# Kernel optimization log

Measured on AMD Instinct MI355X. Metric: run time of the kernel, lower is better.

Reference implementation:

```python
import jax, jax.numpy as jnp
import numpy as np

H, D = 4, 32            # heads, per-head dim (hidden = H*D = 128)
HID = H * D
OUT = 64
NC, ND, E = 50000, 50000, 400000
FC, FD = 256, 256


def setup_inputs() -> dict:
    key = jax.random.key(0)
    ks = iter(jax.random.split(key, 64))

    def n(shape, s=0.05):
        return jax.random.normal(next(ks), shape, dtype=jnp.float32) * s

    def ei(n_src, n_dst):
        return jnp.stack([jax.random.randint(next(ks), (E,), 0, n_src),
                          jax.random.randint(next(ks), (E,), 0, n_dst)]).astype(jnp.int32)

    inp = {
        'x_concept': n((NC, FC), 1.0),
        'x_doc': n((ND, FD), 1.0),
        'ei_cc': ei(NC, NC),
        'ei_dc': ei(ND, NC),
        'ei_cd': ei(NC, ND),
        # conv1 params
        'W1c': n((FC, HID)), 'b1c': n((HID,)),
        'W1d': n((FD, HID)), 'b1d': n((HID,)),
        'a1s_cc': n((H, D)), 'a1d_cc': n((H, D)),
        'a1s_dc': n((H, D)), 'a1d_dc': n((H, D)),
        'a1s_cd': n((H, D)), 'a1d_cd': n((H, D)),
        'k1W': n((HID, HID)), 'k1b': n((HID,)), 'q1': n((HID,)),
        # conv2 params
        'W2c': n((HID, HID)), 'b2c': n((HID,)),
        'W2d': n((HID, HID)), 'b2d': n((HID,)),
        'a2s_cc': n((H, D)), 'a2d_cc': n((H, D)),
        'a2s_dc': n((H, D)), 'a2d_dc': n((H, D)),
        'a2s_cd': n((H, D)), 'a2d_cd': n((H, D)),
        'k2W': n((HID, HID)), 'k2b': n((HID,)), 'q2': n((HID,)),
        # final projection
        'pW': n((HID, OUT)), 'pb': n((OUT,)),
    }
    return inp


def _seg_softmax(logit, idx, n):
    # PyG softmax: exp(x - max_per_segment) / (sum_per_segment + 1e-16)
    m = jax.ops.segment_max(logit, idx, num_segments=n)
    e = jnp.exp(logit - m[idx])
    s = jax.ops.segment_sum(e, idx, num_segments=n)
    return e / (s[idx] + 1e-16)


def _edge_att(h_src, h_dst, a_s, a_d, src, dst, n_dst):
    # h_src: [Ns,H,D]; GAT-style per-edge attention, softmax over dst
    logit = jax.nn.leaky_relu((h_src * a_s).sum(-1)[src] + (h_dst * a_d).sum(-1)[dst], 0.2)
    alpha = _seg_softmax(logit, dst, n_dst)                     # [E,H]
    out = jax.ops.segment_sum(h_src[src] * alpha[:, :, None], dst, num_segments=n_dst)
    return jax.nn.relu(out.reshape(n_dst, H * D))


def _group(outs, kW, kb, q):
    # semantic attention across relation types
    stk = jnp.stack(outs)                                       # [T,N,C]
    score = (q * jnp.tanh(stk @ kW + kb).mean(axis=1)).sum(-1)  # [T]
    w = jax.nn.softmax(score)
    return jnp.einsum('t,tnc->nc', w, stk)


def _han_layer(xc, xd, Wc, bc, Wd, bd, as_cc, ad_cc, as_dc, ad_dc, as_cd, ad_cd,
               kW, kb, q, ei_cc, ei_dc, ei_cd):
    hc = (xc @ Wc + bc).reshape(-1, H, D)
    hd = (xd @ Wd + bd).reshape(-1, H, D)
    nc, nd = hc.shape[0], hd.shape[0]
    o_cc = _edge_att(hc, hc, as_cc, ad_cc, ei_cc[0], ei_cc[1], nc)
    o_dc = _edge_att(hd, hc, as_dc, ad_dc, ei_dc[0], ei_dc[1], nc)
    o_cd = _edge_att(hc, hd, as_cd, ad_cd, ei_cd[0], ei_cd[1], nd)
    return _group([o_cc, o_dc], kW, kb, q), _group([o_cd], kW, kb, q)


def reference(x_concept, x_doc, ei_cc, ei_dc, ei_cd,
              W1c, b1c, W1d, b1d, a1s_cc, a1d_cc, a1s_dc, a1d_dc, a1s_cd, a1d_cd, k1W, k1b, q1,
              W2c, b2c, W2d, b2d, a2s_cc, a2d_cc, a2s_dc, a2d_dc, a2s_cd, a2d_cd, k2W, k2b, q2,
              pW, pb):
    c, d = _han_layer(x_concept, x_doc, W1c, b1c, W1d, b1d,
                      a1s_cc, a1d_cc, a1s_dc, a1d_dc, a1s_cd, a1d_cd,
                      k1W, k1b, q1, ei_cc, ei_dc, ei_cd)
    c, d = jax.nn.elu(c), jax.nn.elu(d)
    c, d = _han_layer(c, d, W2c, b2c, W2d, b2d,
                      a2s_cc, a2d_cc, a2s_dc, a2d_dc, a2s_cd, a2d_cd,
                      k2W, k2b, q2, ei_cc, ei_dc, ei_cd)
    c, d = jax.nn.elu(c), jax.nn.elu(d)
    pc = c @ pW + pb
    pd = d @ pW + pb
    # F.normalize(p=2) on 'concept' only
    pc = pc / jnp.maximum(jnp.linalg.norm(pc, axis=-1, keepdims=True), 1e-12)
    return pc, pd
```

## Files before the change

### kernel.cpp

```cpp
#include <hip/hip_runtime.h>
#include <hip/hip_fp16.h>
#include <cmath>

#define DEVI static __device__ __forceinline__

constexpr int HIDn = 128, OUTn = 64;
constexpr int NCn = 50000, NDn = 50000, En = 400000;
constexpr int SCAN_N = 150000, SCAN_BLK = 1024;
constexpr int SCAN_NB = (SCAN_N + SCAN_BLK - 1) / SCAN_BLK;

typedef __attribute__((ext_vector_type(8))) short bf16x8;
typedef __attribute__((ext_vector_type(4))) float f32x4;

DEVI unsigned fmap(float f) {
  int i = __float_as_int(f);
  return (i < 0) ? ~((unsigned)i) : (((unsigned)i) | 0x80000000u);
}
DEVI float fdecode(unsigned u) {
  int i = (u & 0x80000000u) ? (int)(u & 0x7fffffffu) : (int)(~u);
  return __int_as_float(i);
}

DEVI float tanh_fast(float x) {
  float e = __expf(2.f * x);
  return 1.f - __fdividef(2.f, e + 1.f);
}

DEVI unsigned short f2bf(float x) {
  unsigned u = __float_as_uint(x);
  return (unsigned short)((u + 0x7FFFu + ((u >> 16) & 1u)) >> 16);
}
DEVI float bf2f(unsigned short h) {
  unsigned u = ((unsigned)h) << 16;
  return __uint_as_float(u);
}

template<int MODE, int HALF>
DEVI void loadrow8(float* __restrict__ tmp,
                   const void* __restrict__ A, const void* __restrict__ A2,
                   float w2, float w3, size_t base)
{
  float v[8];
  if (HALF) {
    float4 raw = *(const float4*)((const __half*)A + base);
    const __half2* h2 = (const __half2*)&raw;
    #pragma unroll
    for (int j = 0; j < 4; ++j) {
      float2 f = __half22float2(h2[j]);
      v[2 * j] = f.x; v[2 * j + 1] = f.y;
    }
  } else {
    const float4* p = (const float4*)((const float*)A + base);
    float4 u0 = p[0], u1 = p[1];
    v[0] = u0.x; v[1] = u0.y; v[2] = u0.z; v[3] = u0.w;
    v[4] = u1.x; v[5] = u1.y; v[6] = u1.z; v[7] = u1.w;
  }
  if (MODE == 2) {
    float vb[8];
    if (HALF) {
      float4 raw = *(const float4*)((const __half*)A2 + base);
      const __half2* h2 = (const __half2*)&raw;
      #pragma unroll
      for (int j = 0; j < 4; ++j) {
        float2 f = __half22float2(h2[j]);
        vb[2 * j] = f.x; vb[2 * j + 1] = f.y;
      }
    } else {
      const float4* q = (const float4*)((const float*)A2 + base);
      float4 t0 = q[0], t1 = q[1];
      vb[0] = t0.x; vb[1] = t0.y; vb[2] = t0.z; vb[3] = t0.w;
      vb[4] = t1.x; vb[5] = t1.y; vb[6] = t1.z; vb[7] = t1.w;
    }
    #pragma unroll
    for (int i = 0; i < 8; ++i) v[i] = w2 * v[i] + w3 * vb[i];
  }
  if (MODE >= 1) {
    #pragma unroll
    for (int i = 0; i < 8; ++i) v[i] = (v[i] > 0.f) ? v[i] : (__expf(v[i]) - 1.f);
  }
  #pragma unroll
  for (int i = 0; i < 8; ++i) tmp[i] = v[i];
}

template<int MODE, int HALF>
DEVI bf16x8 packrow8(const void* __restrict__ A, const void* __restrict__ A2,
                     float w2, float w3, size_t base)
{
  float t[8];
  loadrow8<MODE, HALF>(t, A, A2, w2, w3, base);
  bf16x8 r;
  #pragma unroll
  for (int i = 0; i < 8; ++i) r[i] = (short)f2bf(t[i]);
  return r;
}

template<int KI, int MODEc, int MODEd, int IN16, int OUT16>
__global__ __launch_bounds__(256)
void gemm2_mfma(const void* __restrict__ Ac, const void* __restrict__ Ac2,
                const float* __restrict__ wv,
                const unsigned short* __restrict__ WcH, const unsigned short* __restrict__ WcL,
                const float* __restrict__ bc, void* __restrict__ Cc,
                const void* __restrict__ Ad,
                const unsigned short* __restrict__ WdH, const unsigned short* __restrict__ WdL,
                const float* __restrict__ bd, void* __restrict__ Cd,
                int N,
                const float* __restrict__ avc0, const float* __restrict__ avc1,
                const float* __restrict__ avc2, const float* __restrict__ avc3,
                const float* __restrict__ avd0, const float* __restrict__ avd1,
                float* __restrict__ doc0, float* __restrict__ doc1,
                float* __restrict__ doc2, float* __restrict__ doc3,
                float* __restrict__ dod0, float* __restrict__ dod1)
{
  __shared__ float As[64][44];
  __shared__ unsigned short BhS[4096];
  __shared__ unsigned short BlS[4096];
  constexpr int NC = KI / 32;
  const bool isC = (blockIdx.y == 0);
  const void* A  = isC ? Ac : Ad;
  const void* A2 = isC ? Ac2 : nullptr;
  const unsigned short* WH = isC ? WcH : WdH;
  const unsigned short* WL = isC ? WcL : WdL;
  const float* bias = isC ? bc : bd;
  void* Cv = isC ? Cc : Cd;
  float w2 = 0.f, w3 = 0.f;
  if (MODEc == 2) { if (isC) { w2 = wv[2]; w3 = wv[3]; } }

  const int tid = threadIdx.x;
  const int w = tid >> 6, lane = tid & 63;
  const int m = lane & 15, b4 = lane >> 4;
  const int row0 = blockIdx.x * 64;
  const int row0w = row0 + w * 16;

  const int rA = tid >> 2, kqA = (tid & 3) << 3;
  const int rowA = row0 + rA;

  f32x4 acc[8];
  #pragma unroll
  for (int t = 0; t < 8; ++t) acc[t] = (f32x4){0.f, 0.f, 0.f, 0.f};

  float tA[8];
  float4 rbh0, rbh1, rbl0, rbl1;

  auto loadA = [&](int k0) {
    if (rowA < N) {
      if (isC) loadrow8<MODEc, IN16>(tA, A, A2, w2, w3, (size_t)rowA * KI + k0 + kqA);
      else     loadrow8<MODEd, IN16>(tA, A, nullptr, 0.f, 0.f, (size_t)rowA * KI + k0 + kqA);
    } else {
      #pragma unroll
      for (int i = 0; i < 8; ++i) tA[i] = 0.f;
    }
  };
  auto loadB = [&](int c) {
    const float4* ph = (const float4*)(WH + (size_t)c * 4096 + tid * 16);
    const float4* pl = (const float4*)(WL + (size_t)c * 4096 + tid * 16);
    rbh0 = ph[0]; rbh1 = ph[1];
    rbl0 = pl[0]; rbl1 = pl[1];
  };

  loadA(0);
  loadB(0);

  for (int c = 0; c < NC; ++c) {
    *(float4*)&As[rA][kqA]     = make_float4(tA[0], tA[1], tA[2], tA[3]);
    *(float4*)&As[rA][kqA + 4] = make_float4(tA[4], tA[5], tA[6], tA[7]);
    *(float4*)&BhS[tid * 16]     = rbh0;
    *(float4*)&BhS[tid * 16 + 8] = rbh1;
    *(float4*)&BlS[tid * 16]     = rbl0;
    *(float4*)&BlS[tid * 16 + 8] = rbl1;

    if (c + 1 < NC) { loadA((c + 1) * 32); loadB(c + 1); }
    __syncthreads();

    bf16x8 ah, al;
    {
      const float* ap = &As[w * 16 + m][b4 * 8];
      float4 u0 = *(const float4*)ap;
      float4 u1 = *(const float4*)(ap + 4);
      float t8[8] = {u0.x, u0.y, u0.z, u0.w, u1.x, u1.y, u1.z, u1.w};
      #pragma unroll
      for (int i = 0; i < 8; ++i) {
        unsigned short h = f2bf(t8[i]);
        ah[i] = (short)h;
        al[i] = (short)f2bf(t8[i] - bf2f(h));
      }
    }
    #pragma unroll
    for (int t = 0; t < 8; ++t) {
      const int fi = (t * 64 + lane) * 8;
      bf16x8 bh = *(const bf16x8*)&BhS[fi];
      bf16x8 bl = *(const bf16x8*)&BlS[fi];
      acc[t] = __builtin_amdgcn_mfma_f32_16x16x32_bf16(ah, bh, acc[t], 0, 0, 0);
      acc[t] = __builtin_amdgcn_mfma_f32_16x16x32_bf16(al, bh, acc[t], 0, 0, 0);
      acc[t] = __builtin_amdgcn_mfma_f32_16x16x32_bf16(ah, bl, acc[t], 0, 0, 0);
    }
    __syncthreads();
  }

  float bt[8];
  #pragma unroll
  for (int t = 0; t < 8; ++t) bt[t] = bias[t * 16 + m];

  #pragma unroll
  for (int t = 0; t < 8; ++t) {
    const int col = t * 16 + m;
    #pragma unroll
    for (int r = 0; r < 4; ++r) {
      const int row = row0w + b4 * 4 + r;
      if (row < N) {
        float v = acc[t][r] + bt[t];
        if (OUT16) ((__half*)Cv)[(size_t)row * 128 + col] = __float2half(v);
        else       ((float*)Cv)[(size_t)row * 128 + col] = v;
      }
    }
  }

  const float* avp[4];
  float* dop[4];
  int nv;
  if (isC) {
    avp[0] = avc0; avp[1] = avc1; avp[2] = avc2; avp[3] = avc3;
    dop[0] = doc0; dop[1] = doc1; dop[2] = doc2; dop[3] = doc3; nv = 4;
  } else {
    avp[0] = avd0; avp[1] = avd1; avp[2] = avd0; avp[3] = avd1;
    dop[0] = dod0; dop[1] = dod1; dop[2] = dod0; dop[3] = dod1; nv = 2;
  }
  float avv[4][8];
  #pragma unroll
  for (int v = 0; v < 4; ++v) {
    if (v < nv) {
      #pragma unroll
      for (int t = 0; t < 8; ++t) avv[v][t] = avp[v][t * 16 + m];
    }
  }
  #pragma unroll
  for (int h = 0; h < 4; ++h) {
    #pragma unroll
    for (int v = 0; v < 4; ++v) {
      if (v < nv) {
        #pragma unroll
        for (int r = 0; r < 4; ++r) {
          float p = (acc[2 * h][r] + bt[2 * h]) * avv[v][2 * h]
                  + (acc[2 * h + 1][r] + bt[2 * h + 1]) * avv[v][2 * h + 1];
          p += __shfl_xor(p, 1);
          p += __shfl_xor(p, 2);
          p += __shfl_xor(p, 4);
          p += __shfl_xor(p, 8);
          if (m == 0) {
            const int row = row0w + b4 * 4 + r;
            if (row < N) dop[v][(size_t)row * 4 + h] = p;
          }
        }
      }
    }
  }
}

__global__ void hist3(const int* __restrict__ ei0, const int* __restrict__ ei1,
                      const int* __restrict__ ei2, int* __restrict__ deg)
{
  int gid = blockIdx.x * blockDim.x + threadIdx.x;
  if (gid >= 3 * En) return;
  int g = gid / En, e = gid - g * En;
  const int* ei = (g == 0) ? ei0 : (g == 1) ? ei1 : ei2;
  atomicAdd(&deg[g * 50000 + ei[En + e]], 1);
}

__global__ void scan_pass1(const int* __restrict__ deg, int* __restrict__ incl,
                           int* __restrict__ bsum)
{
  __shared__ int wsum[16];
  int tid = threadIdx.x;
  int gid = blockIdx.x * SCAN_BLK + tid;
  int v = (gid < SCAN_N) ? deg[gid] : 0;
  int lane = tid & 63, w = tid >> 6;
  int x = v;
  #pragma unroll
  for (int off = 1; off < 64; off <<= 1) {
    int y = __shfl_up(x, off);
    if (lane >= off) x += y;
  }
  if (lane == 63) wsum[w] = x;
  __syncthreads();
  if (tid == 0) {
    int s = 0;
    #pragma unroll
    for (int ww = 0; ww < 16; ++ww) { int t = wsum[ww]; wsum[ww] = s; s += t; }
    bsum[blockIdx.x] = s;
  }
  __syncthreads();
  x += wsum[w];
  if (gid < SCAN_N) incl[gid] = x;
}

__global__ void scan_pass2(int* __restrict__ bsum, int nb)
{
  __shared__ int wsum[16];
  int tid = threadIdx.x;
  int v = (tid < nb) ? bsum[tid] : 0;
  int lane = tid & 63, w = tid >> 6;
  int x = v;
  #pragma unroll
  for (int off = 1; off < 64; off <<= 1) {
    int y = __shfl_up(x, off);
    if (lane >= off) x += y;
  }
  if (lane == 63) wsum[w] = x;
  __syncthreads();
  if (tid == 0) {
    int s = 0;
    #pragma unroll
    for (int ww = 0; ww < 16; ++ww) { int t = wsum[ww]; wsum[ww] = s; s += t; }
  }
  __syncthreads();
  x += wsum[w];
  if (tid < nb) bsum[tid] = x - v;
}

__global__ void scan_pass3(const int* __restrict__ incl, const int* __restrict__ bsum,
                           int* __restrict__ offs)
{
  int gid = blockIdx.x * SCAN_BLK + threadIdx.x;
  if (gid == 0) offs[0] = 0;
  if (gid < SCAN_N) offs[gid + 1] = incl[gid] + bsum[gid / SCAN_BLK];
}

__global__ void fill3(const int* __restrict__ ei0, const int* __restrict__ ei1,
                      const int* __restrict__ ei2, const int* __restrict__ offs,
                      int* __restrict__ cursor, int* __restrict__ elist)
{
  int gid = blockIdx.x * blockDim.x + threadIdx.x;
  if (gid >= 3 * En) return;
  int g = gid / En, e = gid - g * En;
  const int* ei = (g == 0) ? ei0 : (g == 1) ? ei1 : ei2;
  int s = ei[e], d = g * 50000 + ei[En + e];
  int p = atomicAdd(&cursor[d], 1);
  elist[offs[d] + p] = s;
}

__global__ void wprep(const float* __restrict__ k1W, const float* __restrict__ k2W,
                      const float* __restrict__ pW,
                      const float* __restrict__ W1c, const float* __restrict__ W1d,
                      const float* __restrict__ W2c, const float* __restrict__ W2d,
                      unsigned short* kW1t, unsigned short* kW2t, unsigned short* pWt,
                      unsigned short* W1cH, unsigned short* W1cL,
                      unsigned short* W1dH, unsigned short* W1dL,
                      unsigned short* W2cH, unsigned short* W2cL,
                      unsigned short* W2dH, unsigned short* W2dL)
{
  int gid = blockIdx.x * 256 + threadIdx.x;
  if (gid < 16384) {
    int i = gid, k = i >> 7, col = i & 127;
    int ks = k >> 5, b4 = (k >> 3) & 3, j = k & 7, t = col >> 4, m = col & 15;
    kW1t[(size_t)(((t * 4 + ks) * 64) + m + 16 * b4) * 8 + j] = f2bf(k1W[i]);
  } else if (gid < 32768) {
    int i = gid - 16384, k = i >> 7, col = i & 127;
    int ks = k >> 5, b4 = (k >> 3) & 3, j = k & 7, t = col >> 4, m = col & 15;
    kW2t[(size_t)(((t * 4 + ks) * 64) + m + 16 * b4) * 8 + j] = f2bf(k2W[i]);
  } else if (gid < 40960) {
    int i = gid - 32768, k = i / 64, col = i - k * 64;
    int ks = k >> 5, b4 = (k >> 3) & 3, j = k & 7, t = col >> 4, m = col & 15;
    pWt[(size_t)(((t * 4 + ks) * 64) + m + 16 * b4) * 8 + j] = f2bf(pW[i]);
  } else if (gid < 73728) {
    int i = gid - 40960, k = i >> 7, col = i & 127;
    int c = k >> 5, b4 = (k >> 3) & 3, j = k & 7, t = col >> 4, m = col & 15;
    size_t f = (size_t)(((c * 8 + t) * 64) + m + 16 * b4) * 8 + j;
    float v = W1c[i]; unsigned short h = f2bf(v);
    W1cH[f] = h; W1cL[f] = f2bf(v - bf2f(h));
  } else if (gid < 106496) {
    int i = gid - 73728, k = i >> 7, col = i & 127;
    int c = k >> 5, b4 = (k >> 3) & 3, j = k & 7, t = col >> 4, m = col & 15;
    size_t f = (size_t)(((c * 8 + t) * 64) + m + 16 * b4) * 8 + j;
    float v = W1d[i]; unsigned short h = f2bf(v);
    W1dH[f] = h; W1dL[f] = f2bf(v - bf2f(h));
  } else if (gid < 122880) {
    int i = gid - 106496, k = i >> 7, col = i & 127;
    int c = k >> 5, b4 = (k >> 3) & 3, j = k & 7, t = col >> 4, m = col & 15;
    size_t f = (size_t)(((c * 8 + t) * 64) + m + 16 * b4) * 8 + j;
    float v = W2c[i]; unsigned short h = f2bf(v);
    W2cH[f] = h; W2cL[f] = f2bf(v - bf2f(h));
  } else if (gid < 139264) {
    int i = gid - 122880, k = i >> 7, col = i & 127;
    int c = k >> 5, b4 = (k >> 3) & 3, j = k & 7, t = col >> 4, m = col & 15;
    size_t f = (size_t)(((c * 8 + t) * 64) + m + 16 * b4) * 8 + j;
    float v = W2d[i]; unsigned short h = f2bf(v);
    W2dH[f] = h; W2dL[f] = f2bf(v - bf2f(h));
  }
}

struct EdgeOp {
  const int* offs; const int* elist;
  const float* sdot; const float* ddot;
  const __half* hsrc; __half* out;
};

DEVI void csr_att_body(const EdgeOp& op, int dst, int lane)
{
  const int i0 = op.offs[dst], i1 = op.offs[dst + 1];
  const int hB = lane >> 4;
  const float ddv = op.ddot[dst * 4 + hB];
  const __half* hsrc = op.hsrc;
  const float* sdot = op.sdot;
  const int* el = op.elist;
  const int wsel = lane & 48;
  float den = 0.f, a0 = 0.f, a1 = 0.f;

  for (int base = i0; base < i1; base += 16) {
    int i = base + (lane & 15);
    int s_ = 0;
    float w = 0.f;
    if (i < i1) {
      s_ = el[i];
      float lv = sdot[s_ * 4 + hB] + ddv;
      lv = fminf(fmaxf(lv, 0.2f * lv), 80.f);
      w = __expf(lv);
    }
    float g = w;
    g += __shfl_xor(g, 1);
    g += __shfl_xor(g, 2);
    g += __shfl_xor(g, 4);
    g += __shfl_xor(g, 8);
    den += g;

    const int rem = min(16, i1 - base);
    int j = 0;
    for (; j + 2 <= rem; j += 2) {
      int sA = __shfl(s_, j);
      int sB = __shfl(s_, j + 1);
      float wA = __shfl(w, wsel | j);
      float wB = __shfl(w, wsel | (j + 1));
      float2 hA = __half22float2(*(const __half2*)(hsrc + (size_t)sA * HIDn + lane * 2));
      float2 hBv = __half22float2(*(const __half2*)(hsrc + (size_t)sB * HIDn + lane * 2));
      a0 += hA.x * wA + hBv.x * wB;
      a1 += hA.y * wA + hBv.y * wB;
    }
    if (j < rem) {
      int sA = __shfl(s_, j);
      float wA = __shfl(w, wsel | j);
      float2 hA = __half22float2(*(const __half2*)(hsrc + (size_t)sA * HIDn + lane * 2));
      a0 += hA.x * wA;
      a1 += hA.y * wA;
    }
  }
  float dinv = __fdividef(1.f, den + 1e-16f);
  __half2 o2 = __floats2half2_rn(fmaxf(a0 * dinv, 0.f), fmaxf(a1 * dinv, 0.f));
  *(__half2*)(op.out + (size_t)dst * HIDn + lane * 2) = o2;
}

__global__ __launch_bounds__(256)
void csr_att3(EdgeOp op0, EdgeOp op1, EdgeOp op2, int Ndst)
{
  int wave = (blockIdx.x * 256 + threadIdx.x) >> 6;
  if (wave >= Ndst) return;
  const int lane = threadIdx.x & 63;
  if (blockIdx.y == 0)      csr_att_body(op0, wave, lane);
  else if (blockIdx.y == 1) csr_att_body(op1, wave, lane);
  else                      csr_att_body(op2, wave, lane);
}

__global__ void edge_logit_max(const int* __restrict__ ei,
                               const float* __restrict__ sdot,
                               const float* __restrict__ ddot,
                               unsigned* __restrict__ m)
{
  int e = blockIdx.x * blockDim.x + threadIdx.x;
  if (e >= En) return;
  int s = ei[e], d = ei[En + e];
  #pragma unroll
  for (int hh = 0; hh < 4; ++hh) {
    float l = sdot[s * 4 + hh] + ddot[d * 4 + hh];
    l = (l > 0.f) ? l : 0.2f * l;
    atomicMax(&m[d * 4 + hh], fmap(l));
  }
}

__global__ void edge_exp_sum(const int* __restrict__ ei,
                             const float* __restrict__ sdot,
                             const float* __restrict__ ddot,
                             const unsigned* __restrict__ m,
                             float* __restrict__ sden,
                             float* __restrict__ ebuf)
{
  int e = blockIdx.x * blockDim.x + threadIdx.x;
  if (e >= En) return;
  int s = ei[e], d = ei[En + e];
  #pragma unroll
  for (int hh = 0; hh < 4; ++hh) {
    float l = sdot[s * 4 + hh] + ddot[d * 4 + hh];
    l = (l > 0.f) ? l : 0.2f * l;
    float ex = expf(fminf(l - fdecode(m[d * 4 + hh]), 0.f));
    ebuf[e * 4 + hh] = ex;
    atomicAdd(&sden[d * 4 + hh], ex);
  }
}

__global__ __launch_bounds__(256)
void edge_scatter(const int* __restrict__ ei, const float* __restrict__ hsrc,
                  const float* __restrict__ ebuf, const float* __restrict__ sden,
                  float* __restrict__ out)
{
  int gid  = blockIdx.x * 256 + threadIdx.x;
  int e    = gid >> 6;
  if (e >= En) return;
  int lane = gid & 63;
  int s = ei[e], d = ei[En + e];
  #pragma unroll
  for (int half = 0; half < 2; ++half) {
    int c  = lane + half * 64;
    int hh = c >> 5;
    float alpha = ebuf[e * 4 + hh] / (sden[d * 4 + hh] + 1e-16f);
    atomicAdd(&out[(size_t)d * HIDn + c], hsrc[(size_t)s * HIDn + c] * alpha);
  }
}

__global__ void relu_k(float* __restrict__ x, int n)
{
  int i = blockIdx.x * blockDim.x + threadIdx.x;
  if (i < n) x[i] = fmaxf(x[i], 0.f);
}

template<int IN16>
__global__ __launch_bounds__(256)
void score_mfma(const void* __restrict__ oA, const void* __restrict__ oB,
                const unsigned short* __restrict__ kWt,
                const float* __restrict__ kb, const float* __restrict__ q,
                int N, float* __restrict__ slots)
{
  __shared__ float partw[4];
  const void* o = blockIdx.y ? oB : oA;
  const int tid = threadIdx.x;
  const int w = tid >> 6, lane = tid & 63;
  const int row0 = (blockIdx.x * 4 + w) * 16;
  const int m = lane & 15, b = lane >> 4;
  const int arow = row0 + m;
  const bool rok = arow < N;
  const bf16x8* WT = (const bf16x8*)kWt;

  const bf16x8 zfr = {0, 0, 0, 0, 0, 0, 0, 0};
  bf16x8 afr[4];
  {
    const size_t base = (size_t)arow * 128;
    #pragma unroll
    for (int ks = 0; ks < 4; ++ks) {
      if (rok) afr[ks] = packrow8<0, IN16>(o, nullptr, 0.f, 0.f, base + ks * 32 + b * 8);
      else     afr[ks] = zfr;
    }
  }

  float sum = 0.f;
  #pragma unroll
  for (int t = 0; t < 8; ++t) {
    f32x4 acc = {0.f, 0.f, 0.f, 0.f};
    const int col = t * 16 + m;
    #pragma unroll
    for (int ks = 0; ks < 4; ++ks)
      acc = __builtin_amdgcn_mfma_f32_16x16x32_bf16(afr[ks], WT[(t * 4 + ks) * 64 + lane], acc, 0, 0, 0);
    const float qc = q[col], kbc = kb[col];
    #pragma unroll
    for (int r = 0; r < 4; ++r) {
      int row = row0 + b * 4 + r;
      if (row < N) sum += qc * tanh_fast(acc[r] + kbc);
    }
  }
  #pragma unroll
  for (int off = 32; off > 0; off >>= 1) sum += __shfl_down(sum, off);
  if (lane == 0) partw[w] = sum;
  __syncthreads();
  if (tid == 0)
    atomicAdd(&slots[blockIdx.y],
              (partw[0] + partw[1] + partw[2] + partw[3]) * (1.f / (float)N));
}

__global__ void softmax2_kernel(float* sb)
{
  float s0 = sb[0], s1 = sb[1];
  float mx = fmaxf(s0, s1);
  float e0 = expf(s0 - mx), e1 = expf(s1 - mx);
  float inv = 1.f / (e0 + e1);
  sb[2] = e0 * inv;
  sb[3] = e1 * inv;
}

template<int IN16>
__global__ __launch_bounds__(256)
void proj2_mfma(const void* __restrict__ fa, const void* __restrict__ fb,
                const float* __restrict__ wv, const void* __restrict__ fd,
                const unsigned short* __restrict__ pWt, const float* __restrict__ pb,
                float* __restrict__ outc, float* __restrict__ outd, int N)
{
  const bool isC = (blockIdx.y == 0);
  const int tid = threadIdx.x;
  const int w = tid >> 6, lane = tid & 63;
  const int row0 = (blockIdx.x * 4 + w) * 16;
  const int m = lane & 15, b = lane >> 4;
  const int arow = row0 + m;
  const bool rok = arow < N;
  float* out = isC ? outc : outd;
  const bf16x8* WT = (const bf16x8*)pWt;

  const bf16x8 zfr = {0, 0, 0, 0, 0, 0, 0, 0};
  bf16x8 afr[4];
  {
    const size_t base = (size_t)arow * 128;
    if (isC) {
      const float w2 = wv[2], w3 = wv[3];
      #pragma unroll
      for (int ks = 0; ks < 4; ++ks) {
        if (rok) afr[ks] = packrow8<2, IN16>(fa, fb, w2, w3, base + ks * 32 + b * 8);
        else     afr[ks] = zfr;
      }
    } else {
      #pragma unroll
      for (int ks = 0; ks < 4; ++ks) {
        if (rok) afr[ks] = packrow8<1, IN16>(fd, nullptr, 0.f, 0.f, base + ks * 32 + b * 8);
        else     afr[ks] = zfr;
      }
    }
  }

  f32x4 accs[4];
  float pbc[4];
  #pragma unroll
  for (int t = 0; t < 4; ++t) {
    f32x4 acc = {0.f, 0.f, 0.f, 0.f};
    const int col = t * 16 + m;
    #pragma unroll
    for (int ks = 0; ks < 4; ++ks)
      acc = __builtin_amdgcn_mfma_f32_16x16x32_bf16(afr[ks], WT[(t * 4 + ks) * 64 + lane], acc, 0, 0, 0);
    accs[t] = acc;
    pbc[t] = pb[col];
  }

  #pragma unroll
  for (int r = 0; r < 4; ++r) {
    const int row = row0 + b * 4 + r;
    float v[4];
    #pragma unroll
    for (int t = 0; t < 4; ++t) v[t] = accs[t][r] + pbc[t];
    if (isC) {
      float ss = v[0]*v[0] + v[1]*v[1] + v[2]*v[2] + v[3]*v[3];
      ss += __shfl_xor(ss, 1);
      ss += __shfl_xor(ss, 2);
      ss += __shfl_xor(ss, 4);
      ss += __shfl_xor(ss, 8);
      float inv = 1.f / fmaxf(sqrtf(ss), 1e-12f);
      #pragma unroll
      for (int t = 0; t < 4; ++t) v[t] *= inv;
    }
    if (row < N) {
      #pragma unroll
      for (int t = 0; t < 4; ++t)
        out[(size_t)row * OUTn + t * 16 + m] = v[t];
    }
  }
}

static void run_edge_fb(hipStream_t stream, const int* ei,
                        const float* sdot, const float* ddot, const float* hsrc,
                        float* outb, int Ndst,
                        unsigned* mbuf, float* sden, float* ebuf)
{
  hipMemsetAsync(mbuf, 0, (size_t)Ndst * 4 * sizeof(unsigned), stream);
  edge_logit_max<<<(En + 255) / 256, 256, 0, stream>>>(ei, sdot, ddot, mbuf);
  hipMemsetAsync(sden, 0, (size_t)Ndst * 4 * sizeof(float), stream);
  edge_exp_sum<<<(En + 255) / 256, 256, 0, stream>>>(ei, sdot, ddot, mbuf, sden, ebuf);
  hipMemsetAsync(outb, 0, (size_t)Ndst * HIDn * sizeof(float), stream);
  edge_scatter<<<((size_t)En * 64 + 255) / 256, 256, 0, stream>>>(ei, hsrc, ebuf, sden, outb);
  relu_k<<<((size_t)Ndst * HIDn + 255) / 256, 256, 0, stream>>>(outb, Ndst * HIDn);
}

extern "C" void kernel_launch(void* const* d_in, const int* in_sizes, int n_in,
                              void* d_out, int out_size, void* d_ws, size_t ws_size,
                              hipStream_t stream)
{
  const float* xc    = (const float*)d_in[0];
  const float* xd    = (const float*)d_in[1];
  const int*   ei_cc = (const int*)d_in[2];
  const int*   ei_dc = (const int*)d_in[3];
  const int*   ei_cd = (const int*)d_in[4];
  const float* W1c = (const float*)d_in[5];  const float* b1c = (const float*)d_in[6];
  const float* W1d = (const float*)d_in[7];  const float* b1d = (const float*)d_in[8];
  const float* a1s_cc = (const float*)d_in[9];  const float* a1d_cc = (const float*)d_in[10];
  const float* a1s_dc = (const float*)d_in[11]; const float* a1d_dc = (const float*)d_in[12];
  const float* a1s_cd = (const float*)d_in[13]; const float* a1d_cd = (const float*)d_in[14];
  const float* k1W = (const float*)d_in[15]; const float* k1b = (const float*)d_in[16];
  const float* q1  = (const float*)d_in[17];
  const float* W2c = (const float*)d_in[18]; const float* b2c = (const float*)d_in[19];
  const float* W2d = (const float*)d_in[20]; const float* b2d = (const float*)d_in[21];
  const float* a2s_cc = (const float*)d_in[22]; const float* a2d_cc = (const float*)d_in[23];
  const float* a2s_dc = (const float*)d_in[24]; const float* a2d_dc = (const float*)d_in[25];
  const float* a2s_cd = (const float*)d_in[26]; const float* a2d_cd = (const float*)d_in[27];
  const float* k2W = (const float*)d_in[28]; const float* k2b = (const float*)d_in[29];
  const float* q2  = (const float*)d_in[30];
  const float* pW  = (const float*)d_in[31]; const float* pb  = (const float*)d_in[32];

  float* ws = (float*)d_ws;
  const size_t NB = (size_t)NCn * HIDn;
  float* B0 = ws;
  float* B1 = ws + NB;
  float* B2 = ws + 2 * NB;
  float* B3 = ws + 3 * NB;
  float* B4 = ws + 4 * NB;
  float* sml = ws + 5 * NB;
  float* scc = sml;
  float* dcc = sml + 200000;
  float* ddc = sml + 400000;
  float* scd = sml + 600000;
  float* sdc = sml + 800000;
  float* dcd = sml + 1000000;
  float* scoreB = sml + 1200000;
  float* R0 = sml + 1200016;
  int*  R0i = (int*)R0;
  int*  offsBase  = R0i;
  int*  elistBase = R0i + 150004;
  int*  degBase   = R0i + 1350004;
  int*  cursorBase= R0i + 1500004;
  int*  inclBase  = R0i + 1650004;
  int*  bsumBase  = R0i + 1800004;
  unsigned short* kW1t = (unsigned short*)(R0i + 1801028);
  unsigned short* kW2t = (unsigned short*)(R0i + 1809220);
  unsigned short* pWt  = (unsigned short*)(R0i + 1817412);
  unsigned short* W1cH = (unsigned short*)(R0i + 1821508);
  unsigned short* W1cL = (unsigned short*)(R0i + 1837892);
  unsigned short* W1dH = (unsigned short*)(R0i + 1854276);
  unsigned short* W1dL = (unsigned short*)(R0i + 1870660);
  unsigned short* W2cH = (unsigned short*)(R0i + 1887044);
  unsigned short* W2cL = (unsigned short*)(R0i + 1895236);
  unsigned short* W2dH = (unsigned short*)(R0i + 1903428);
  unsigned short* W2dL = (unsigned short*)(R0i + 1911620);
  unsigned* mbuf = (unsigned*)R0;
  float*    sden = R0 + 200000;
  float*    ebuf = R0 + 400000;

  const size_t REQ_FLOATS = 5 * NB + 1200016 + 1919812;
  const bool useCsr = ws_size >= REQ_FLOATS * sizeof(float);

  if (useCsr) {
    hipMemsetAsync(degBase, 0, 300000 * sizeof(int), stream);
    hist3<<<(3 * En + 255) / 256, 256, 0, stream>>>(ei_cc, ei_dc, ei_cd, degBase);
    scan_pass1<<<SCAN_NB, SCAN_BLK, 0, stream>>>(degBase, inclBase, bsumBase);
    scan_pass2<<<1, SCAN_BLK, 0, stream>>>(bsumBase, SCAN_NB);
    scan_pass3<<<SCAN_NB, SCAN_BLK, 0, stream>>>(inclBase, bsumBase, offsBase);
    fill3<<<(3 * En + 255) / 256, 256, 0, stream>>>(ei_cc, ei_dc, ei_cd,
                                                    offsBase, cursorBase, elistBase);
  }
  wprep<<<(139264 + 255) / 256, 256, 0, stream>>>(k1W, k2W, pW, W1c, W1d, W2c, W2d,
                                                  kW1t, kW2t, pWt,
                                                  W1cH, W1cL, W1dH, W1dL,
                                                  W2cH, W2cL, W2dH, W2dL);

  hipMemsetAsync(scoreB, 0, 8 * sizeof(float), stream);

  const int NT64 = (NCn + 63) / 64;
  const int* offs0 = offsBase;
  const int* offs1 = offsBase + 50000;
  const int* offs2 = offsBase + 100000;

  auto edge_layer = [&](void* hc, void* hd, void* oCC, void* oDC, void* oCD) {
    if (useCsr) {
      EdgeOp o0{offs0, elistBase, scc, dcc, (const __half*)hc, (__half*)oCC};
      EdgeOp o1{offs1, elistBase, sdc, ddc, (const __half*)hd, (__half*)oDC};
      EdgeOp o2{offs2, elistBase, scd, dcd, (const __half*)hc, (__half*)oCD};
      csr_att3<<<dim3((NCn + 3) / 4, 3), 256, 0, stream>>>(o0, o1, o2, NCn);
    } else {
      run_edge_fb(stream, ei_cc, scc, dcc, (const float*)hc, (float*)oCC, NCn, mbuf, sden, ebuf);
      run_edge_fb(stream, ei_dc, sdc, ddc, (const float*)hd, (float*)oDC, NCn, mbuf, sden, ebuf);
      run_edge_fb(stream, ei_cd, scd, dcd, (const float*)hc, (float*)oCD, NDn, mbuf, sden, ebuf);
    }
  };

  if (useCsr) {
    gemm2_mfma<256, 0, 0, 0, 1><<<dim3(NT64, 2), 256, 0, stream>>>(
        xc, nullptr, nullptr, W1cH, W1cL, b1c, B0,
        xd, W1dH, W1dL, b1d, B1, NCn,
        a1s_cc, a1d_cc, a1d_dc, a1s_cd, a1s_dc, a1d_cd,
        scc, dcc, ddc, scd, sdc, dcd);
    edge_layer(B0, B1, B2, B3, B4);
    score_mfma<1><<<dim3(NT64, 2), 256, 0, stream>>>(B2, B3, kW1t, k1b, q1, NCn, scoreB);
    softmax2_kernel<<<1, 1, 0, stream>>>(scoreB);

    gemm2_mfma<128, 2, 1, 1, 1><<<dim3(NT64, 2), 256, 0, stream>>>(
        B2, B3, scoreB, W2cH, W2cL, b2c, B0,
        B4, W2dH, W2dL, b2d, B1, NCn,
        a2s_cc, a2d_cc, a2d_dc, a2s_cd, a2s_dc, a2d_cd,
        scc, dcc, ddc, scd, sdc, dcd);
    edge_layer(B0, B1, B2, B3, B4);
    score_mfma<1><<<dim3(NT64, 2), 256, 0, stream>>>(B2, B3, kW2t, k2b, q2, NCn, scoreB + 4);
    softmax2_kernel<<<1, 1, 0, stream>>>(scoreB + 4);

    proj2_mfma<1><<<dim3(NT64, 2), 256, 0, stream>>>(B2, B3, scoreB + 4, B4, pWt, pb,
                                                     (float*)d_out,
                                                     (float*)d_out + (size_t)NCn * OUTn, NCn);
  } else {
    gemm2_mfma<256, 0, 0, 0, 0><<<dim3(NT64, 2), 256, 0, stream>>>(
        xc, nullptr, nullptr, W1cH, W1cL, b1c, B0,
        xd, W1dH, W1dL, b1d, B1, NCn,
        a1s_cc, a1d_cc, a1d_dc, a1s_cd, a1s_dc, a1d_cd,
        scc, dcc, ddc, scd, sdc, dcd);
    edge_layer(B0, B1, B2, B3, B4);
    score_mfma<0><<<dim3(NT64, 2), 256, 0, stream>>>(B2, B3, kW1t, k1b, q1, NCn, scoreB);
    softmax2_kernel<<<1, 1, 0, stream>>>(scoreB);

    gemm2_mfma<128, 2, 1, 0, 0><<<dim3(NT64, 2), 256, 0, stream>>>(
        B2, B3, scoreB, W2cH, W2cL, b2c, B0,
        B4, W2dH, W2dL, b2d, B1, NCn,
        a2s_cc, a2d_cc, a2d_dc, a2s_cd, a2s_dc, a2d_cd,
        scc, dcc, ddc, scd, sdc, dcd);
    edge_layer(B0, B1, B2, B3, B4);
    score_mfma<0><<<dim3(NT64, 2), 256, 0, stream>>>(B2, B3, kW2t, k2b, q2, NCn, scoreB + 4);
    softmax2_kernel<<<1, 1, 0, stream>>>(scoreB + 4);

    proj2_mfma<0><<<dim3(NT64, 2), 256, 0, stream>>>(B2, B3, scoreB + 4, B4, pWt, pb,
                                                     (float*)d_out,
                                                     (float*)d_out + (size_t)NCn * OUTn, NCn);
  }
}
```

Baseline: 443.1 us.

## Double GEMM row tile to 128 rows per block to reuse weight tiles

```diff
diff --git a/kernel.cpp b/kernel.cpp
--- a/kernel.cpp
+++ b/kernel.cpp
@@ -111,7 +111,7 @@
                 float* __restrict__ doc2, float* __restrict__ doc3,
                 float* __restrict__ dod0, float* __restrict__ dod1)
 {
-  __shared__ float As[64][44];
+  __shared__ float As[128][44];
   __shared__ unsigned short BhS[4096];
   __shared__ unsigned short BlS[4096];
   constexpr int NC = KI / 32;
@@ -128,26 +128,37 @@
   const int tid = threadIdx.x;
   const int w = tid >> 6, lane = tid & 63;
   const int m = lane & 15, b4 = lane >> 4;
-  const int row0 = blockIdx.x * 64;
-  const int row0w = row0 + w * 16;
-
-  const int rA = tid >> 2, kqA = (tid & 3) << 3;
-  const int rowA = row0 + rA;
-
-  f32x4 acc[8];
-  #pragma unroll
-  for (int t = 0; t < 8; ++t) acc[t] = (f32x4){0.f, 0.f, 0.f, 0.f};
-
-  float tA[8];
+  const int row0 = blockIdx.x * 128;
+  const int row0w = row0 + w * 32;
+
+  const int rA0 = tid >> 2, kqA = (tid & 3) << 3;
+  const int rA1 = rA0 + 64;
+  const int rowA0 = row0 + rA0;
+  const int rowA1 = row0 + rA1;
+
+  f32x4 acc[2][8];
+  #pragma unroll
+  for (int rt = 0; rt < 2; ++rt)
+    #pragma unroll
+    for (int t = 0; t < 8; ++t) acc[rt][t] = (f32x4){0.f, 0.f, 0.f, 0.f};
+
+  float tA[16];
   float4 rbh0, rbh1, rbl0, rbl1;
 
   auto loadA = [&](int k0) {
-    if (rowA < N) {
-      if (isC) loadrow8<MODEc, IN16>(tA, A, A2, w2, w3, (size_t)rowA * KI + k0 + kqA);
-      else     loadrow8<MODEd, IN16>(tA, A, nullptr, 0.f, 0.f, (size_t)rowA * KI + k0 + kqA);
+    if (rowA0 < N) {
+      if (isC) loadrow8<MODEc, IN16>(tA, A, A2, w2, w3, (size_t)rowA0 * KI + k0 + kqA);
+      else     loadrow8<MODEd, IN16>(tA, A, nullptr, 0.f, 0.f, (size_t)rowA0 * KI + k0 + kqA);
     } else {
       #pragma unroll
       for (int i = 0; i < 8; ++i) tA[i] = 0.f;
+    }
+    if (rowA1 < N) {
+      if (isC) loadrow8<MODEc, IN16>(tA + 8, A, A2, w2, w3, (size_t)rowA1 * KI + k0 + kqA);
+      else     loadrow8<MODEd, IN16>(tA + 8, A, nullptr, 0.f, 0.f, (size_t)rowA1 * KI + k0 + kqA);
+    } else {
+      #pragma unroll
+      for (int i = 0; i < 8; ++i) tA[8 + i] = 0.f;
     }
   };
   auto loadB = [&](int c) {
@@ -161,8 +172,10 @@
   loadB(0);
 
   for (int c = 0; c < NC; ++c) {
-    *(float4*)&As[rA][kqA]     = make_float4(tA[0], tA[1], tA[2], tA[3]);
-    *(float4*)&As[rA][kqA + 4] = make_float4(tA[4], tA[5], tA[6], tA[7]);
+    *(float4*)&As[rA0][kqA]     = make_float4(tA[0], tA[1], tA[2], tA[3]);
+    *(float4*)&As[rA0][kqA + 4] = make_float4(tA[4], tA[5], tA[6], tA[7]);
+    *(float4*)&As[rA1][kqA]     = make_float4(tA[8], tA[9], tA[10], tA[11]);
+    *(float4*)&As[rA1][kqA + 4] = make_float4(tA[12], tA[13], tA[14], tA[15]);
     *(float4*)&BhS[tid * 16]     = rbh0;
     *(float4*)&BhS[tid * 16 + 8] = rbh1;
     *(float4*)&BlS[tid * 16]     = rbl0;
@@ -171,17 +184,29 @@
     if (c + 1 < NC) { loadA((c + 1) * 32); loadB(c + 1); }
     __syncthreads();
 
-    bf16x8 ah, al;
+    bf16x8 ah0, al0, ah1, al1;
     {
-      const float* ap = &As[w * 16 + m][b4 * 8];
+      const float* ap = &As[row0w - row0 + m][b4 * 8];
       float4 u0 = *(const float4*)ap;
       float4 u1 = *(const float4*)(ap + 4);
       float t8[8] = {u0.x, u0.y, u0.z, u0.w, u1.x, u1.y, u1.z, u1.w};
       #pragma unroll
       for (int i = 0; i < 8; ++i) {
         unsigned short h = f2bf(t8[i]);
-        ah[i] = (short)h;
-        al[i] = (short)f2bf(t8[i] - bf2f(h));
+        ah0[i] = (short)h;
+        al0[i] = (short)f2bf(t8[i] - bf2f(h));
+      }
+    }
+    {
+      const float* ap = &As[row0w - row0 + 16 + m][b4 * 8];
+      float4 u0 = *(const float4*)ap;
+      float4 u1 = *(const float4*)(ap + 4);
+      float t8[8] = {u0.x, u0.y, u0.z, u0.w, u1.x, u1.y, u1.z, u1.w};
+      #pragma unroll
+      for (int i = 0; i < 8; ++i) {
+        unsigned short h = f2bf(t8[i]);
+        ah1[i] = (short)h;
+        al1[i] = (short)f2bf(t8[i] - bf2f(h));
       }
     }
     #pragma unroll
@@ -189,9 +214,12 @@
       const int fi = (t * 64 + lane) * 8;
       bf16x8 bh = *(const bf16x8*)&BhS[fi];
       bf16x8 bl = *(const bf16x8*)&BlS[fi];
-      acc[t] = __builtin_amdgcn_mfma_f32_16x16x32_bf16(ah, bh, acc[t], 0, 0, 0);
-      acc[t] = __builtin_amdgcn_mfma_f32_16x16x32_bf16(al, bh, acc[t], 0, 0, 0);
-      acc[t] = __builtin_amdgcn_mfma_f32_16x16x32_bf16(ah, bl, acc[t], 0, 0, 0);
+      acc[0][t] = __builtin_amdgcn_mfma_f32_16x16x32_bf16(ah0, bh, acc[0][t], 0, 0, 0);
+      acc[0][t] = __builtin_amdgcn_mfma_f32_16x16x32_bf16(al0, bh, acc[0][t], 0, 0, 0);
+      acc[0][t] = __builtin_amdgcn_mfma_f32_16x16x32_bf16(ah0, bl, acc[0][t], 0, 0, 0);
+      acc[1][t] = __builtin_amdgcn_mfma_f32_16x16x32_bf16(ah1, bh, acc[1][t], 0, 0, 0);
+      acc[1][t] = __builtin_amdgcn_mfma_f32_16x16x32_bf16(al1, bh, acc[1][t], 0, 0, 0);
+      acc[1][t] = __builtin_amdgcn_mfma_f32_16x16x32_bf16(ah1, bl, acc[1][t], 0, 0, 0);
     }
     __syncthreads();
   }
@@ -201,15 +229,18 @@
   for (int t = 0; t < 8; ++t) bt[t] = bias[t * 16 + m];
 
   #pragma unroll
-  for (int t = 0; t < 8; ++t) {
-    const int col = t * 16 + m;
-    #pragma unroll
-    for (int r = 0; r < 4; ++r) {
-      const int row = row0w + b4 * 4 + r;
-      if (row < N) {
-        float v = acc[t][r] + bt[t];
-        if (OUT16) ((__half*)Cv)[(size_t)row * 128 + col] = __float2half(v);
-        else       ((float*)Cv)[(size_t)row * 128 + col] = v;
+  for (int rt = 0; rt < 2; ++rt) {
+    #pragma unroll
+    for (int t = 0; t < 8; ++t) {
+      const int col = t * 16 + m;
+      #pragma unroll
+      for (int r = 0; r < 4; ++r) {
+        const int row = row0w + rt * 16 + b4 * 4 + r;
+        if (row < N) {
+          float v = acc[rt][t][r] + bt[t];
+          if (OUT16) ((__half*)Cv)[(size_t)row * 128 + col] = __float2half(v);
+          else       ((float*)Cv)[(size_t)row * 128 + col] = v;
+        }
       }
     }
   }
@@ -233,21 +264,24 @@
     }
   }
   #pragma unroll
-  for (int h = 0; h < 4; ++h) {
-    #pragma unroll
-    for (int v = 0; v < 4; ++v) {
-      if (v < nv) {
-        #pragma unroll
-        for (int r = 0; r < 4; ++r) {
-          float p = (acc[2 * h][r] + bt[2 * h]) * avv[v][2 * h]
-                  + (acc[2 * h + 1][r] + bt[2 * h + 1]) * avv[v][2 * h + 1];
-          p += __shfl_xor(p, 1);
-          p += __shfl_xor(p, 2);
-          p += __shfl_xor(p, 4);
-          p += __shfl_xor(p, 8);
-          if (m == 0) {
-            const int row = row0w + b4 * 4 + r;
-            if (row < N) dop[v][(size_t)row * 4 + h] = p;
+  for (int rt = 0; rt < 2; ++rt) {
+    #pragma unroll
+    for (int h = 0; h < 4; ++h) {
+      #pragma unroll
+      for (int v = 0; v < 4; ++v) {
+        if (v < nv) {
+          #pragma unroll
+          for (int r = 0; r < 4; ++r) {
+            float p = (acc[rt][2 * h][r] + bt[2 * h]) * avv[v][2 * h]
+                    + (acc[rt][2 * h + 1][r] + bt[2 * h + 1]) * avv[v][2 * h + 1];
+            p += __shfl_xor(p, 1);
+            p += __shfl_xor(p, 2);
+            p += __shfl_xor(p, 4);
+            p += __shfl_xor(p, 8);
+            if (m == 0) {
+              const int row = row0w + rt * 16 + b4 * 4 + r;
+              if (row < N) dop[v][(size_t)row * 4 + h] = p;
+            }
           }
         }
       }
@@ -751,6 +785,7 @@
   hipMemsetAsync(scoreB, 0, 8 * sizeof(float), stream);
 
   const int NT64 = (NCn + 63) / 64;
+  const int NT128 = (NCn + 127) / 128;
   const int* offs0 = offsBase;
   const int* offs1 = offsBase + 50000;
   const int* offs2 = offsBase + 100000;
@@ -769,7 +804,7 @@
   };
 
   if (useCsr) {
-    gemm2_mfma<256, 0, 0, 0, 1><<<dim3(NT64, 2), 256, 0, stream>>>(
+    gemm2_mfma<256, 0, 0, 0, 1><<<dim3(NT128, 2), 256, 0, stream>>>(
         xc, nullptr, nullptr, W1cH, W1cL, b1c, B0,
         xd, W1dH, W1dL, b1d, B1, NCn,
         a1s_cc, a1d_cc, a1d_dc, a1s_cd, a1s_dc, a1d_cd,
@@ -778,7 +813,7 @@
     score_mfma<1><<<dim3(NT64, 2), 256, 0, stream>>>(B2, B3, kW1t, k1b, q1, NCn, scoreB);
     softmax2_kernel<<<1, 1, 0, stream>>>(scoreB);
 
-    gemm2_mfma<128, 2, 1, 1, 1><<<dim3(NT64, 2), 256, 0, stream>>>(
+    gemm2_mfma<128, 2, 1, 1, 1><<<dim3(NT128, 2), 256, 0, stream>>>(
         B2, B3, scoreB, W2cH, W2cL, b2c, B0,
         B4, W2dH, W2dL, b2d, B1, NCn,
         a2s_cc, a2d_cc, a2d_dc, a2s_cd, a2s_dc, a2d_cd,
@@ -791,7 +826,7 @@
                                                      (float*)d_out,
                                                      (float*)d_out + (size_t)NCn * OUTn, NCn);
   } else {
-    gemm2_mfma<256, 0, 0, 0, 0><<<dim3(NT64, 2), 256, 0, stream>>>(
+    gemm2_mfma<256, 0, 0, 0, 0><<<dim3(NT128, 2), 256, 0, stream>>>(
         xc, nullptr, nullptr, W1cH, W1cL, b1c, B0,
         xd, W1dH, W1dL, b1d, B1, NCn,
         a1s_cc, a1d_cc, a1d_dc, a1s_cd, a1s_dc, a1d_cd,
@@ -800,7 +835,7 @@
     score_mfma<0><<<dim3(NT64, 2), 256, 0, stream>>>(B2, B3, kW1t, k1b, q1, NCn, scoreB);
     softmax2_kernel<<<1, 1, 0, stream>>>(scoreB);
 
-    gemm2_mfma<128, 2, 1, 0, 0><<<dim3(NT64, 2), 256, 0, stream>>>(
+    gemm2_mfma<128, 2, 1, 0, 0><<<dim3(NT128, 2), 256, 0, stream>>>(
         B2, B3, scoreB, W2cH, W2cL, b2c, B0,
         B4, W2dH, W2dL, b2d, B1, NCn,
         a2s_cc, a2d_cc, a2d_dc, a2s_cd, a2s_dc, a2d_cd,
```

Measured after the change: 487.4 us. 10.0% more time.

## Gather source rows with 16-byte loads, four edges per wave step

Applied to the files above, without the earlier changes.

```diff
diff --git a/kernel.cpp b/kernel.cpp
--- a/kernel.cpp
+++ b/kernel.cpp
@@ -396,54 +396,65 @@
 DEVI void csr_att_body(const EdgeOp& op, int dst, int lane)
 {
   const int i0 = op.offs[dst], i1 = op.offs[dst + 1];
-  const int hB = lane >> 4;
-  const float ddv = op.ddot[dst * 4 + hB];
+  const int g  = lane >> 4;
+  const int l  = lane & 15;
+  const int hc = l >> 2;
+  const float ddv = op.ddot[dst * 4 + g];
   const __half* hsrc = op.hsrc;
   const float* sdot = op.sdot;
   const int* el = op.elist;
-  const int wsel = lane & 48;
-  float den = 0.f, a0 = 0.f, a1 = 0.f;
+  float den = 0.f;
+  float acc[8] = {0.f, 0.f, 0.f, 0.f, 0.f, 0.f, 0.f, 0.f};
 
   for (int base = i0; base < i1; base += 16) {
-    int i = base + (lane & 15);
+    int i = base + l;
     int s_ = 0;
     float w = 0.f;
     if (i < i1) {
       s_ = el[i];
-      float lv = sdot[s_ * 4 + hB] + ddv;
+      float lv = sdot[s_ * 4 + g] + ddv;
       lv = fminf(fmaxf(lv, 0.2f * lv), 80.f);
       w = __expf(lv);
     }
-    float g = w;
-    g += __shfl_xor(g, 1);
-    g += __shfl_xor(g, 2);
-    g += __shfl_xor(g, 4);
-    g += __shfl_xor(g, 8);
-    den += g;
+    float gs = w;
+    gs += __shfl_xor(gs, 1);
+    gs += __shfl_xor(gs, 2);
+    gs += __shfl_xor(gs, 4);
+    gs += __shfl_xor(gs, 8);
+    den += gs;
 
     const int rem = min(16, i1 - base);
-    int j = 0;
-    for (; j + 2 <= rem; j += 2) {
-      int sA = __shfl(s_, j);
-      int sB = __shfl(s_, j + 1);
-      float wA = __shfl(w, wsel | j);
-      float wB = __shfl(w, wsel | (j + 1));
-      float2 hA = __half22float2(*(const __half2*)(hsrc + (size_t)sA * HIDn + lane * 2));
-      float2 hBv = __half22float2(*(const __half2*)(hsrc + (size_t)sB * HIDn + lane * 2));
-      a0 += hA.x * wA + hBv.x * wB;
-      a1 += hA.y * wA + hBv.y * wB;
-    }
-    if (j < rem) {
-      int sA = __shfl(s_, j);
-      float wA = __shfl(w, wsel | j);
-      float2 hA = __half22float2(*(const __half2*)(hsrc + (size_t)sA * HIDn + lane * 2));
-      a0 += hA.x * wA;
-      a1 += hA.y * wA;
-    }
-  }
-  float dinv = __fdividef(1.f, den + 1e-16f);
-  __half2 o2 = __floats2half2_rn(fmaxf(a0 * dinv, 0.f), fmaxf(a1 * dinv, 0.f));
-  *(__half2*)(op.out + (size_t)dst * HIDn + lane * 2) = o2;
+    const int nk = (rem + 3) >> 2;
+    for (int k = 0; k < nk; ++k) {
+      const int j = g + 4 * k;
+      int sj = __shfl(s_, j);
+      float wj = __shfl(w, hc * 16 + j);
+      float4 hv = *(const float4*)(hsrc + (size_t)sj * HIDn + l * 8);
+      const __half2* h2 = (const __half2*)&hv;
+      #pragma unroll
+      for (int q = 0; q < 4; ++q) {
+        float2 f = __half22float2(h2[q]);
+        acc[2 * q]     += f.x * wj;
+        acc[2 * q + 1] += f.y * wj;
+      }
+    }
+  }
+
+  #pragma unroll
+  for (int q = 0; q < 8; ++q) {
+    acc[q] += __shfl_xor(acc[q], 16);
+    acc[q] += __shfl_xor(acc[q], 32);
+  }
+  float dv = __shfl(den, hc * 16);
+  float dinv = __fdividef(1.f, dv + 1e-16f);
+  if (lane < 16) {
+    __half2 o[4];
+    #pragma unroll
+    for (int q = 0; q < 4; ++q)
+      o[q] = __floats2half2_rn(fmaxf(acc[2 * q] * dinv, 0.f),
+                               fmaxf(acc[2 * q + 1] * dinv, 0.f));
+    *(float4*)(op.out + (size_t)dst * HIDn + l * 8) = *(const float4*)o;
+  }
 }
 
 __global__ __launch_bounds__(256)
```

Result: faster. 427.9 us (-3.4%).
